# Optimization experiments

Measured on AMD Instinct MI355X. Metric: run time of the kernel, lower is better.

The kernel has to match this reference:

```python
import jax, jax.numpy as jnp
import numpy as np

P = 3          # graph partitions
CO = 64        # out_channels
KS = 9         # temporal kernel size (Gamma)
STRIDE = 1     # temporal stride
EPS = 1e-3     # keras BatchNormalization default epsilon


def setup_inputs() -> dict:
    key = jax.random.key(0)
    k1, k2, k3 = jax.random.split(key, 3)
    x = jax.random.normal(k1, (32, 64, 300, 25), dtype=jnp.float32)      # (N, C_in, L, V)
    A = jax.random.uniform(k2, (3, 25, 25), dtype=jnp.float32)           # (P, V, V)
    W = jax.random.normal(k3, (64, 192), dtype=jnp.float32) * 0.05       # (C_in, C_out*P)
    gamma = jnp.ones((64,), dtype=jnp.float32)
    beta = jnp.zeros((64,), dtype=jnp.float32)
    mean = jnp.zeros((64,), dtype=jnp.float32)
    var = jnp.ones((64,), dtype=jnp.float32)
    return {"x": x, "A": A, "W": W, "gamma": gamma, "beta": beta, "mean": mean, "var": var}


def _lt_matrix(L):
    # sum of shifted identities: lt[r, r + i*STRIDE] = 1 for i in [0, KS//STRIDE)
    lt = jnp.zeros((L, L), dtype=jnp.float32)
    for i in range(KS // STRIDE):
        lt = lt + jnp.eye(L, k=i * STRIDE, dtype=jnp.float32)
    return lt


def reference(x, A, W, gamma, beta, mean, var):
    N, C, L, V = x.shape
    res = x  # identity residual (in_channels == out_channels, stride == 1)
    # 1x1 conv: (N,C,L,V) x (C, CO*P) -> (N, CO*P, L, V); channel k = c*P + p (split into CO groups of P)
    y = jnp.einsum('nclv,ck->nklv', x, W)
    y = y.reshape(N, CO, P, L, V)  # (N, C_out, P, L, V)
    # partitioned graph matmul over joints: contract V with A[p]
    z = jnp.einsum('ncplv,pvw->ncplw', y, A)
    # temporal aggregation via handcrafted banded matrix, then sum over partitions
    lt = _lt_matrix(L)
    t = jnp.einsum('ncplv,lm->ncmv', z, lt)  # partition sum fused into einsum
    # BN (inference) over channel axis + ReLU
    inv = gamma / jnp.sqrt(var + EPS)
    xn = (t - mean[None, :, None, None]) * inv[None, :, None, None] + beta[None, :, None, None]
    xn = jax.nn.relu(xn)
    # residual add + final ReLU (dropout is identity at inference)
    return jax.nn.relu(xn + res)
```

## Files before the change

### kernel.cpp

```cpp
#include <hip/hip_runtime.h>
#include <cstdint>
#include <cstddef>

typedef short bf16x8 __attribute__((ext_vector_type(8)));
typedef float f32x4 __attribute__((ext_vector_type(4)));

#define EPS 1e-3f
#define AT_OFF 13312

__device__ __forceinline__ short f32_to_bf16s(float f) {
    union { float f; uint32_t u; } v; v.f = f;
    return (short)((v.u + 0x7FFFu + ((v.u >> 16) & 1u)) >> 16);
}

__global__ __launch_bounds__(256) void prep_kernel(const float* __restrict__ A,
                                                   const float* __restrict__ W,
                                                   unsigned short* __restrict__ wt,
                                                   unsigned short* __restrict__ at) {
    int idx = blockIdx.x * 256 + threadIdx.x;
    if (idx < 12288) {
        int kp = idx >> 6, ci = idx & 63;
        wt[idx] = (unsigned short)f32_to_bf16s(W[ci * 192 + kp]);
    } else {
        int j = idx - 12288;
        if (j < 3072) {
            int w = j / 96, k = j - w * 96;
            float val = 0.f;
            if (w < 25 && k < 75) {
                int p = k / 25, v = k - p * 25;
                val = A[(p * 25 + v) * 25 + w];
            }
            at[j] = (unsigned short)f32_to_bf16s(val);
        }
    }
}

__device__ __forceinline__ void load_a1(int g, const unsigned short* __restrict__ wt,
                                        int lcol, int q, bf16x8 (&a1)[3][2]) {
    #pragma unroll
    for (int mt = 0; mt < 3; ++mt)
        #pragma unroll
        for (int s = 0; s < 2; ++s)
            a1[mt][s] = *(const bf16x8*)(wt + (size_t)(g * 48 + mt * 16 + lcol) * 64 + 32 * s + 8 * q);
}

__device__ __forceinline__ void do_group(int g, bool loadNext, int gnext,
    const unsigned short* __restrict__ wt, short* smem,
    const bf16x8 (&a1)[3][2], bf16x8 (&a1n)[3][2], const bf16x8 (&b1)[2][2],
    const float* __restrict__ x, float* __restrict__ out,
    const float* scs, const float* shs,
    size_t outrow, int lg, int wv, int q, int lcol)
{
    f32x4 acc[3][2];
    #pragma unroll
    for (int mt = 0; mt < 3; ++mt)
        #pragma unroll
        for (int nt = 0; nt < 2; ++nt) acc[mt][nt] = (f32x4){0.f, 0.f, 0.f, 0.f};
    #pragma unroll
    for (int s = 0; s < 2; ++s)
        #pragma unroll
        for (int mt = 0; mt < 3; ++mt) {
            bf16x8 av = a1[mt][s];
            #pragma unroll
            for (int nt = 0; nt < 2; ++nt)
                acc[mt][nt] = __builtin_amdgcn_mfma_f32_16x16x32_bf16(av, b1[nt][s], acc[mt][nt], 0, 0, 0);
        }

    float res[2][4];
    #pragma unroll
    for (int nt = 0; nt < 2; ++nt) {
        int w = nt * 16 + lcol;
        bool val = (w < 25) && (lg < 300);
        #pragma unroll
        for (int r = 0; r < 4; ++r) {
            int c = g * 16 + 4 * q + r;
            res[nt][r] = val ? x[outrow + (size_t)c * 7500 + w] : 0.f;
        }
    }

    #pragma unroll
    for (int mt = 0; mt < 3; ++mt)
        #pragma unroll
        for (int nt = 0; nt < 2; ++nt) {
            int v = nt * 16 + lcol;
            if (v < 25) {
                #pragma unroll
                for (int r = 0; r < 4; ++r) {
                    int kpl = mt * 16 + 4 * q + r;
                    int cl = kpl / 3, p = kpl - 3 * cl;
                    smem[(wv * 16 + cl) * 104 + 25 * p + v] = f32_to_bf16s(acc[mt][nt][r]);
                }
            }
        }

    if (loadNext) load_a1(gnext, wt, lcol, q, a1n);

    bf16x8 b2l[2][3];
    #pragma unroll
    for (int nt = 0; nt < 2; ++nt)
        #pragma unroll
        for (int s = 0; s < 3; ++s)
            b2l[nt][s] = *(const bf16x8*)&smem[AT_OFF + (nt * 16 + lcol) * 104 + 32 * s + 8 * q];

    f32x4 c0 = {0.f, 0.f, 0.f, 0.f}, c1 = {0.f, 0.f, 0.f, 0.f};
    #pragma unroll
    for (int s = 0; s < 3; ++s) {
        bf16x8 a2 = *(const bf16x8*)&smem[(wv * 16 + lcol) * 104 + 32 * s + 8 * q];
        c0 = __builtin_amdgcn_mfma_f32_16x16x32_bf16(a2, b2l[0][s], c0, 0, 0, 0);
        c1 = __builtin_amdgcn_mfma_f32_16x16x32_bf16(a2, b2l[1][s], c1, 0, 0, 0);
    }

    if (lg < 300) {
        #pragma unroll
        for (int nt = 0; nt < 2; ++nt) {
            int w = nt * 16 + lcol;
            if (w < 25) {
                f32x4 cc = nt ? c1 : c0;
                #pragma unroll
                for (int r = 0; r < 4; ++r) {
                    int c = g * 16 + 4 * q + r;
                    float o = fmaxf(cc[r] * scs[c] + shs[c], 0.f);
                    out[outrow + (size_t)c * 7500 + w] = fmaxf(o + res[nt][r], 0.f);
                }
            }
        }
    }
}

__global__ __launch_bounds__(512, 4) void mega_kernel(
    const float* __restrict__ x,
    const unsigned short* __restrict__ wt,
    const unsigned short* __restrict__ at,
    const float* __restrict__ gamma, const float* __restrict__ beta,
    const float* __restrict__ mean, const float* __restrict__ var,
    float* __restrict__ out) {
    const int lin = blockIdx.x + 38 * blockIdx.y;
    const int logical = (lin & 7) * 152 + (lin >> 3);
    const int ch = logical % 38;
    const int n  = logical / 38;

    const int l0 = ch * 8;
    const int tid = threadIdx.x;
    const int wv = tid >> 6, lane = tid & 63, q = lane >> 4, lcol = lane & 15;

    __shared__ __align__(16) short smem[16640];
    __shared__ float scs[64], shs[64];

    const int aw = tid >> 4, aj = (tid & 15) * 6;
    const uint32_t* asrc = (const uint32_t*)(at + aw * 96 + aj);
    uint32_t av0 = asrc[0], av1 = asrc[1], av2 = asrc[2];
    __builtin_amdgcn_sched_barrier(0);

    if (tid < 64) {
        float sc = gamma[tid] * rsqrtf(var[tid] + EPS);
        scs[tid] = sc;
        shs[tid] = beta[tid] - mean[tid] * sc;
    }

    #pragma unroll 1
    for (int rep = 0; rep < 4; ++rep) {
        int cidx = tid + rep * 512;
        if (cidx < 1600) {
            int ci = cidx / 25, v = cidx - ci * 25;
            const float* xp = x + (size_t)(n * 64 + ci) * 7500 + v;
            float vals[16];
            #pragma unroll
            for (int i = 0; i < 16; ++i) {
                int l = l0 - 8 + i;
                vals[i] = (l >= 0 && l < 300) ? xp[l * 25] : 0.f;
            }
            float run = vals[0] + vals[1] + vals[2] + vals[3]
                      + vals[4] + vals[5] + vals[6] + vals[7];
            short* wb = &smem[(ci >> 3) * 1656 + (ci & 7)];
            #pragma unroll
            for (int j = 0; j < 8; ++j) {
                run += vals[j + 8];
                wb[(j * 25 + v) * 8] = f32_to_bf16s(run);
                run -= vals[j];
            }
        }
    }

    {
        uint32_t* adst = (uint32_t*)&smem[AT_OFF + aw * 104 + aj];
        adst[0] = av0; adst[1] = av1; adst[2] = av2;
    }
    __syncthreads();

    bf16x8 b1[2][2];
    #pragma unroll
    for (int nt = 0; nt < 2; ++nt) {
        int col = wv * 25 + nt * 16 + lcol;
        #pragma unroll
        for (int s = 0; s < 2; ++s)
            b1[nt][s] = *(const bf16x8*)&smem[(4 * s + q) * 1656 + col * 8];
    }
    __syncthreads();

    #pragma unroll
    for (int i = lane; i < 512; i += 64) {
        int r = i >> 5, cc = 72 + (i & 31);
        smem[(wv * 16 + r) * 104 + cc] = 0;
    }

    const int lg = l0 + wv;
    const size_t outrow = ((size_t)n * 64 * 300 + lg) * 25;

    bf16x8 a1a[3][2], a1b[3][2];
    load_a1(0, wt, lcol, q, a1a);
    do_group(0, true,  1, wt, smem, a1a, a1b, b1, x, out, scs, shs, outrow, lg, wv, q, lcol);
    __builtin_amdgcn_sched_barrier(0);
    do_group(1, true,  2, wt, smem, a1b, a1a, b1, x, out, scs, shs, outrow, lg, wv, q, lcol);
    __builtin_amdgcn_sched_barrier(0);
    do_group(2, true,  3, wt, smem, a1a, a1b, b1, x, out, scs, shs, outrow, lg, wv, q, lcol);
    __builtin_amdgcn_sched_barrier(0);
    do_group(3, false, 3, wt, smem, a1b, a1a, b1, x, out, scs, shs, outrow, lg, wv, q, lcol);
}

extern "C" void kernel_launch(void* const* d_in, const int* in_sizes, int n_in,
                              void* d_out, int out_size, void* d_ws, size_t ws_size,
                              hipStream_t stream) {
    const float* x     = (const float*)d_in[0];
    const float* A     = (const float*)d_in[1];
    const float* W     = (const float*)d_in[2];
    const float* gamma = (const float*)d_in[3];
    const float* beta  = (const float*)d_in[4];
    const float* mean  = (const float*)d_in[5];
    const float* var   = (const float*)d_in[6];
    float* out = (float*)d_out;

    char* ws = (char*)d_ws;
    unsigned short* wt = (unsigned short*)ws;
    unsigned short* at = (unsigned short*)(ws + 24576);

    prep_kernel<<<60, 256, 0, stream>>>(A, W, wt, at);
    mega_kernel<<<dim3(38, 32), 512, 0, stream>>>(x, wt, at, gamma, beta, mean, var, out);
}
```

Measured before the change: 162.7 us.

## Split temporal windowing into separate kernel writing bf16 tiles to workspace

Splits the fused kernel in two. A new window kernel computes the temporal running sums of x as bf16 and writes them to a global workspace, including zero padding. The GEMM kernel then reads its B operand directly from that workspace instead of building it in shared memory, which removes one barrier and the LDS staging. The cost is an extra kernel launch plus a global write and read of about 32 MB of bf16 tiles, against the expected gain of lighter GEMM blocks with better occupancy.

Measured after the change: 182.0 us. 1.12x slower.

```diff
diff --git a/kernel.cpp b/kernel.cpp
--- a/kernel.cpp
+++ b/kernel.cpp
@@ -35,127 +35,16 @@
     }
 }
 
-__device__ __forceinline__ void load_a1(int g, const unsigned short* __restrict__ wt,
-                                        int lcol, int q, bf16x8 (&a1)[3][2]) {
-    #pragma unroll
-    for (int mt = 0; mt < 3; ++mt)
-        #pragma unroll
-        for (int s = 0; s < 2; ++s)
-            a1[mt][s] = *(const bf16x8*)(wt + (size_t)(g * 48 + mt * 16 + lcol) * 64 + 32 * s + 8 * q);
-}
-
-__device__ __forceinline__ void do_group(int g, bool loadNext, int gnext,
-    const unsigned short* __restrict__ wt, short* smem,
-    const bf16x8 (&a1)[3][2], bf16x8 (&a1n)[3][2], const bf16x8 (&b1)[2][2],
-    const float* __restrict__ x, float* __restrict__ out,
-    const float* scs, const float* shs,
-    size_t outrow, int lg, int wv, int q, int lcol)
-{
-    f32x4 acc[3][2];
-    #pragma unroll
-    for (int mt = 0; mt < 3; ++mt)
-        #pragma unroll
-        for (int nt = 0; nt < 2; ++nt) acc[mt][nt] = (f32x4){0.f, 0.f, 0.f, 0.f};
-    #pragma unroll
-    for (int s = 0; s < 2; ++s)
-        #pragma unroll
-        for (int mt = 0; mt < 3; ++mt) {
-            bf16x8 av = a1[mt][s];
-            #pragma unroll
-            for (int nt = 0; nt < 2; ++nt)
-                acc[mt][nt] = __builtin_amdgcn_mfma_f32_16x16x32_bf16(av, b1[nt][s], acc[mt][nt], 0, 0, 0);
-        }
-
-    float res[2][4];
-    #pragma unroll
-    for (int nt = 0; nt < 2; ++nt) {
-        int w = nt * 16 + lcol;
-        bool val = (w < 25) && (lg < 300);
-        #pragma unroll
-        for (int r = 0; r < 4; ++r) {
-            int c = g * 16 + 4 * q + r;
-            res[nt][r] = val ? x[outrow + (size_t)c * 7500 + w] : 0.f;
-        }
-    }
-
-    #pragma unroll
-    for (int mt = 0; mt < 3; ++mt)
-        #pragma unroll
-        for (int nt = 0; nt < 2; ++nt) {
-            int v = nt * 16 + lcol;
-            if (v < 25) {
-                #pragma unroll
-                for (int r = 0; r < 4; ++r) {
-                    int kpl = mt * 16 + 4 * q + r;
-                    int cl = kpl / 3, p = kpl - 3 * cl;
-                    smem[(wv * 16 + cl) * 104 + 25 * p + v] = f32_to_bf16s(acc[mt][nt][r]);
-                }
-            }
-        }
-
-    if (loadNext) load_a1(gnext, wt, lcol, q, a1n);
-
-    bf16x8 b2l[2][3];
-    #pragma unroll
-    for (int nt = 0; nt < 2; ++nt)
-        #pragma unroll
-        for (int s = 0; s < 3; ++s)
-            b2l[nt][s] = *(const bf16x8*)&smem[AT_OFF + (nt * 16 + lcol) * 104 + 32 * s + 8 * q];
-
-    f32x4 c0 = {0.f, 0.f, 0.f, 0.f}, c1 = {0.f, 0.f, 0.f, 0.f};
-    #pragma unroll
-    for (int s = 0; s < 3; ++s) {
-        bf16x8 a2 = *(const bf16x8*)&smem[(wv * 16 + lcol) * 104 + 32 * s + 8 * q];
-        c0 = __builtin_amdgcn_mfma_f32_16x16x32_bf16(a2, b2l[0][s], c0, 0, 0, 0);
-        c1 = __builtin_amdgcn_mfma_f32_16x16x32_bf16(a2, b2l[1][s], c1, 0, 0, 0);
-    }
-
-    if (lg < 300) {
-        #pragma unroll
-        for (int nt = 0; nt < 2; ++nt) {
-            int w = nt * 16 + lcol;
-            if (w < 25) {
-                f32x4 cc = nt ? c1 : c0;
-                #pragma unroll
-                for (int r = 0; r < 4; ++r) {
-                    int c = g * 16 + 4 * q + r;
-                    float o = fmaxf(cc[r] * scs[c] + shs[c], 0.f);
-                    out[outrow + (size_t)c * 7500 + w] = fmaxf(o + res[nt][r], 0.f);
-                }
-            }
-        }
-    }
-}
-
-__global__ __launch_bounds__(512, 4) void mega_kernel(
-    const float* __restrict__ x,
-    const unsigned short* __restrict__ wt,
-    const unsigned short* __restrict__ at,
-    const float* __restrict__ gamma, const float* __restrict__ beta,
-    const float* __restrict__ mean, const float* __restrict__ var,
-    float* __restrict__ out) {
+__global__ __launch_bounds__(512) void window_kernel(const float* __restrict__ x,
+                                                     unsigned short* __restrict__ xw) {
     const int lin = blockIdx.x + 38 * blockIdx.y;
     const int logical = (lin & 7) * 152 + (lin >> 3);
     const int ch = logical % 38;
     const int n  = logical / 38;
-
     const int l0 = ch * 8;
     const int tid = threadIdx.x;
-    const int wv = tid >> 6, lane = tid & 63, q = lane >> 4, lcol = lane & 15;
-
-    __shared__ __align__(16) short smem[16640];
-    __shared__ float scs[64], shs[64];
-
-    const int aw = tid >> 4, aj = (tid & 15) * 6;
-    const uint32_t* asrc = (const uint32_t*)(at + aw * 96 + aj);
-    uint32_t av0 = asrc[0], av1 = asrc[1], av2 = asrc[2];
-    __builtin_amdgcn_sched_barrier(0);
-
-    if (tid < 64) {
-        float sc = gamma[tid] * rsqrtf(var[tid] + EPS);
-        scs[tid] = sc;
-        shs[tid] = beta[tid] - mean[tid] * sc;
-    }
+
+    unsigned short* tile = xw + (size_t)(n * 38 + ch) * 13248;
 
     #pragma unroll 1
     for (int rep = 0; rep < 4; ++rep) {
@@ -171,29 +60,155 @@
             }
             float run = vals[0] + vals[1] + vals[2] + vals[3]
                       + vals[4] + vals[5] + vals[6] + vals[7];
-            short* wb = &smem[(ci >> 3) * 1656 + (ci & 7)];
+            unsigned short* wb = &tile[(ci >> 3) * 1656 + (ci & 7)];
             #pragma unroll
             for (int j = 0; j < 8; ++j) {
                 run += vals[j + 8];
-                wb[(j * 25 + v) * 8] = f32_to_bf16s(run);
+                wb[(j * 25 + v) * 8] = (unsigned short)f32_to_bf16s(run);
                 run -= vals[j];
             }
-        }
-    }
-
-    {
-        uint32_t* adst = (uint32_t*)&smem[AT_OFF + aw * 104 + aj];
-        adst[0] = av0; adst[1] = av1; adst[2] = av2;
-    }
-    __syncthreads();
-
+        } else if (cidx < 2048) {
+            int t = cidx - 1600;
+            if (t < 448) {
+                int oi = t / 56, off = t - oi * 56;
+                tile[oi * 1656 + 1600 + off] = 0;
+            }
+        }
+    }
+}
+
+__device__ __forceinline__ void load_a1(int g, const unsigned short* __restrict__ wt,
+                                        int lcol, int q, bf16x8 (&a1)[3][2]) {
+    #pragma unroll
+    for (int mt = 0; mt < 3; ++mt)
+        #pragma unroll
+        for (int s = 0; s < 2; ++s)
+            a1[mt][s] = *(const bf16x8*)(wt + (size_t)(g * 48 + mt * 16 + lcol) * 64 + 32 * s + 8 * q);
+}
+
+__device__ __forceinline__ void do_group(int g, bool loadNext, int gnext,
+    const unsigned short* __restrict__ wt, short* smem,
+    const bf16x8 (&a1)[3][2], bf16x8 (&a1n)[3][2], const bf16x8 (&b1)[2][2],
+    const float* __restrict__ x, float* __restrict__ out,
+    const float* scs, const float* shs,
+    size_t outrow, int lg, int wv, int q, int lcol)
+{
+    f32x4 acc[3][2];
+    #pragma unroll
+    for (int mt = 0; mt < 3; ++mt)
+        #pragma unroll
+        for (int nt = 0; nt < 2; ++nt) acc[mt][nt] = (f32x4){0.f, 0.f, 0.f, 0.f};
+    #pragma unroll
+    for (int s = 0; s < 2; ++s)
+        #pragma unroll
+        for (int mt = 0; mt < 3; ++mt) {
+            bf16x8 av = a1[mt][s];
+            #pragma unroll
+            for (int nt = 0; nt < 2; ++nt)
+                acc[mt][nt] = __builtin_amdgcn_mfma_f32_16x16x32_bf16(av, b1[nt][s], acc[mt][nt], 0, 0, 0);
+        }
+
+    float res[2][4];
+    #pragma unroll
+    for (int nt = 0; nt < 2; ++nt) {
+        int w = nt * 16 + lcol;
+        bool val = (w < 25) && (lg < 300);
+        #pragma unroll
+        for (int r = 0; r < 4; ++r) {
+            int c = g * 16 + 4 * q + r;
+            res[nt][r] = val ? x[outrow + (size_t)c * 7500 + w] : 0.f;
+        }
+    }
+
+    #pragma unroll
+    for (int mt = 0; mt < 3; ++mt)
+        #pragma unroll
+        for (int nt = 0; nt < 2; ++nt) {
+            int v = nt * 16 + lcol;
+            if (v < 25) {
+                #pragma unroll
+                for (int r = 0; r < 4; ++r) {
+                    int kpl = mt * 16 + 4 * q + r;
+                    int cl = kpl / 3, p = kpl - 3 * cl;
+                    smem[(wv * 16 + cl) * 104 + 25 * p + v] = f32_to_bf16s(acc[mt][nt][r]);
+                }
+            }
+        }
+
+    if (loadNext) load_a1(gnext, wt, lcol, q, a1n);
+
+    bf16x8 b2l[2][3];
+    #pragma unroll
+    for (int nt = 0; nt < 2; ++nt)
+        #pragma unroll
+        for (int s = 0; s < 3; ++s)
+            b2l[nt][s] = *(const bf16x8*)&smem[AT_OFF + (nt * 16 + lcol) * 104 + 32 * s + 8 * q];
+
+    f32x4 c0 = {0.f, 0.f, 0.f, 0.f}, c1 = {0.f, 0.f, 0.f, 0.f};
+    #pragma unroll
+    for (int s = 0; s < 3; ++s) {
+        bf16x8 a2 = *(const bf16x8*)&smem[(wv * 16 + lcol) * 104 + 32 * s + 8 * q];
+        c0 = __builtin_amdgcn_mfma_f32_16x16x32_bf16(a2, b2l[0][s], c0, 0, 0, 0);
+        c1 = __builtin_amdgcn_mfma_f32_16x16x32_bf16(a2, b2l[1][s], c1, 0, 0, 0);
+    }
+
+    if (lg < 300) {
+        #pragma unroll
+        for (int nt = 0; nt < 2; ++nt) {
+            int w = nt * 16 + lcol;
+            if (w < 25) {
+                f32x4 cc = nt ? c1 : c0;
+                #pragma unroll
+                for (int r = 0; r < 4; ++r) {
+                    int c = g * 16 + 4 * q + r;
+                    float o = fmaxf(cc[r] * scs[c] + shs[c], 0.f);
+                    out[outrow + (size_t)c * 7500 + w] = fmaxf(o + res[nt][r], 0.f);
+                }
+            }
+        }
+    }
+}
+
+__global__ __launch_bounds__(512, 4) void gemm_kernel(
+    const float* __restrict__ x,
+    const unsigned short* __restrict__ wt,
+    const unsigned short* __restrict__ at,
+    const unsigned short* __restrict__ xw,
+    const float* __restrict__ gamma, const float* __restrict__ beta,
+    const float* __restrict__ mean, const float* __restrict__ var,
+    float* __restrict__ out) {
+    const int lin = blockIdx.x + 38 * blockIdx.y;
+    const int logical = (lin & 7) * 152 + (lin >> 3);
+    const int ch = logical % 38;
+    const int n  = logical / 38;
+    const int l0 = ch * 8;
+    const int tid = threadIdx.x;
+    const int wv = tid >> 6, lane = tid & 63, q = lane >> 4, lcol = lane & 15;
+
+    __shared__ __align__(16) short smem[16640];
+    __shared__ float scs[64], shs[64];
+
+    const unsigned short* tile = xw + (size_t)(n * 38 + ch) * 13248;
     bf16x8 b1[2][2];
     #pragma unroll
     for (int nt = 0; nt < 2; ++nt) {
         int col = wv * 25 + nt * 16 + lcol;
         #pragma unroll
         for (int s = 0; s < 2; ++s)
-            b1[nt][s] = *(const bf16x8*)&smem[(4 * s + q) * 1656 + col * 8];
+            b1[nt][s] = *(const bf16x8*)&tile[(4 * s + q) * 1656 + col * 8];
+    }
+
+    {
+        const int aw = tid >> 4, aj = (tid & 15) * 6;
+        const uint32_t* asrc = (const uint32_t*)(at + aw * 96 + aj);
+        uint32_t a0 = asrc[0], a1v = asrc[1], a2v = asrc[2];
+        uint32_t* adst = (uint32_t*)&smem[AT_OFF + aw * 104 + aj];
+        adst[0] = a0; adst[1] = a1v; adst[2] = a2v;
+    }
+    if (tid < 64) {
+        float sc = gamma[tid] * rsqrtf(var[tid] + EPS);
+        scs[tid] = sc;
+        shs[tid] = beta[tid] - mean[tid] * sc;
     }
     __syncthreads();
 
@@ -232,7 +247,9 @@
     char* ws = (char*)d_ws;
     unsigned short* wt = (unsigned short*)ws;
     unsigned short* at = (unsigned short*)(ws + 24576);
+    unsigned short* xw = (unsigned short*)(ws + 32768);
 
     prep_kernel<<<60, 256, 0, stream>>>(A, W, wt, at);
-    mega_kernel<<<dim3(38, 32), 512, 0, stream>>>(x, wt, at, gamma, beta, mean, var, out);
-}
+    window_kernel<<<dim3(38, 32), 512, 0, stream>>>(x, xw);
+    gemm_kernel<<<dim3(38, 32), 512, 0, stream>>>(x, wt, at, xw, gamma, beta, mean, var, out);
+}
```
